# Kernel tuning notes

Hardware: AMD Instinct MI355X
Metric: run time of the kernel (lower is better)

## Reference

```python
import jax, jax.numpy as jnp
import numpy as np

N_NODES = 50000
N_EDGES = 600000
CH = 128      # units / channels
RBF = 200     # ceil(cutoff/gap) = ceil(20.0/0.1)
LOG2 = 0.6931471805599453


def shifted_softplus(x):
    # tf.where(x < 14, softplus(where(x < 14, x, 0)), x) - log(2)
    safe = jnp.where(x < 14.0, x, jnp.zeros_like(x))
    return jnp.where(x < 14.0, jax.nn.softplus(safe), x) - LOG2


def _glorot(key, shape):
    fan_in = shape[0] if len(shape) > 1 else shape[0]
    fan_out = shape[-1]
    lim = np.sqrt(6.0 / (fan_in + fan_out))
    return jax.random.uniform(key, shape, jnp.float32, -lim, lim)


def setup_inputs() -> dict:
    key = jax.random.key(0)
    ks = jax.random.split(key, 12)
    rbf = jax.random.uniform(ks[0], (N_EDGES, RBF), jnp.float32)
    x = jax.random.normal(ks[1], (N_NODES, CH), jnp.float32)
    src = jax.random.randint(ks[2], (N_EDGES,), 0, N_NODES, jnp.int32)
    return {
        "rbf": rbf,
        "x": x,
        "src": src,
        "w1": _glorot(ks[3], (RBF, CH)),
        "b1": _glorot(ks[4], (CH,)),
        "w2": _glorot(ks[5], (CH, CH)),
        "b2": _glorot(ks[6], (CH,)),
        "w3": _glorot(ks[7], (CH, CH)),
        "w4": _glorot(ks[8], (CH, CH)),
        "b4": _glorot(ks[9], (CH,)),
        "w5": _glorot(ks[10], (CH, CH)),
        "b5": _glorot(ks[11], (CH,)),
    }


def reference(rbf, x, src, w1, b1, w2, b2, w3, w4, b4, w5, b5):
    # filter-generating MLP on edge RBF features: [E, RBF] -> [E, CH]
    h = shifted_softplus(rbf @ w1 + b1)
    w = shifted_softplus(h @ w2 + b2)
    # node feature transform, gather to edges by SOURCE index
    f = x @ w3                         # [N, CH]
    wf = w * f[src]                    # [E, CH] broadcast_node_to_edges + multiply
    # scatter-sum edges back to SOURCE nodes
    conv = jax.ops.segment_sum(wf, src, num_segments=N_NODES)  # [N, CH]
    # output MLP + residual
    y = shifted_softplus(conv @ w4 + b4)
    v = y @ w5 + b5
    return x + v
```

## Files before the change

kernel.cpp:

```cpp
#include <hip/hip_runtime.h>

#define CH      128
#define RBFD    200
#define NNODES  50000
#define NEDGES  600000
#define LOG2F_  0.6931471805599453f

#define K1P     224
#define RSTR    232
#define HSTR    136

typedef __attribute__((ext_vector_type(8))) __bf16 bf16x8;
typedef __attribute__((ext_vector_type(4))) float  f32x4;

__device__ __forceinline__ float ssp(float x) {
    float sp = (x < 14.0f) ? __logf(1.0f + __expf(x)) : x;
    return sp - LOG2F_;
}

__device__ __forceinline__ unsigned short f2bf(float f) {
    union { float f; unsigned int u; } v; v.f = f;
    unsigned int r = v.u + 0x7FFFu + ((v.u >> 16) & 1u);
    return (unsigned short)(r >> 16);
}

__global__ __launch_bounds__(256) void prep_weights(const float* __restrict__ w1,
                                                    const float* __restrict__ w2,
                                                    unsigned short* __restrict__ w1T,
                                                    unsigned short* __restrict__ w2T) {
    int i = blockIdx.x * 256 + threadIdx.x;
    if (i < 128 * K1P) {
        int n = i / K1P, k = i % K1P;
        w1T[i] = (k < RBFD) ? f2bf(w1[k * CH + n]) : (unsigned short)0;
    } else {
        int j = i - 128 * K1P;
        if (j < 128 * 128) {
            int n = j / 128, k = j % 128;
            w2T[j] = f2bf(w2[k * CH + n]);
        }
    }
}

__global__ __launch_bounds__(256, 3) void edge_kernel(const float* __restrict__ rbf,
                                                      const float* __restrict__ b1,
                                                      const float* __restrict__ b2,
                                                      const int* __restrict__ src,
                                                      const unsigned short* __restrict__ w1T,
                                                      const unsigned short* __restrict__ w2T,
                                                      float* __restrict__ convw) {
    __shared__ unsigned short rbf_s[64 * RSTR];
    __shared__ unsigned short h_s[64 * HSTR];
    const int t = threadIdx.x;
    const int lane = t & 63;
    const int wv = t >> 6;
    const size_t e0 = (size_t)blockIdx.x * 64;

    const int l15 = lane & 15;
    const int lg  = lane >> 4;
    const int col0 = wv * 32 + l15;

    bf16x8 B1[2][7];
#pragma unroll
    for (int nt = 0; nt < 2; nt++) {
        const int row = wv * 32 + nt * 16 + l15;
#pragma unroll
        for (int kt = 0; kt < 7; kt++)
            B1[nt][kt] = *(const bf16x8*)(w1T + (size_t)row * K1P + kt * 32 + lg * 8);
    }

    {
        const float4* g = (const float4*)(rbf + e0 * RBFD);
        for (int i = t; i < 3200; i += 256) {
            float4 v = g[i];
            int row = i / 50, c4 = (i % 50) * 4;
            unsigned short* d = &rbf_s[row * RSTR + c4];
            union { unsigned short s[4]; unsigned long long u; } p;
            p.s[0] = f2bf(v.x); p.s[1] = f2bf(v.y); p.s[2] = f2bf(v.z); p.s[3] = f2bf(v.w);
            *(unsigned long long*)d = p.u;
        }
        for (int i = t; i < 2048; i += 256) {
            int row = i >> 5, k = RBFD + (i & 31);
            rbf_s[row * RSTR + k] = 0;
        }
    }
    __syncthreads();

    const float bias10 = b1[col0];
    const float bias11 = b1[col0 + 16];

#pragma unroll
    for (int m = 0; m < 4; m++) {
        f32x4 acc0 = {0.f, 0.f, 0.f, 0.f};
        f32x4 acc1 = {0.f, 0.f, 0.f, 0.f};
        const unsigned short* abase = &rbf_s[(m * 16 + l15) * RSTR + lg * 8];
#pragma unroll
        for (int kt = 0; kt < 7; kt++) {
            bf16x8 a = *(const bf16x8*)(abase + kt * 32);
            acc0 = __builtin_amdgcn_mfma_f32_16x16x32_bf16(a, B1[0][kt], acc0, 0, 0, 0);
            acc1 = __builtin_amdgcn_mfma_f32_16x16x32_bf16(a, B1[1][kt], acc1, 0, 0, 0);
        }
        const int hrow0 = m * 16 + lg * 4;
#pragma unroll
        for (int r = 0; r < 4; r++) {
            h_s[(hrow0 + r) * HSTR + col0]      = f2bf(ssp(acc0[r] + bias10));
            h_s[(hrow0 + r) * HSTR + col0 + 16] = f2bf(ssp(acc1[r] + bias11));
        }
    }
    __syncthreads();

    bf16x8 B2[2][4];
#pragma unroll
    for (int nt = 0; nt < 2; nt++) {
        const int row = wv * 32 + nt * 16 + l15;
#pragma unroll
        for (int kt = 0; kt < 4; kt++)
            B2[nt][kt] = *(const bf16x8*)(w2T + (size_t)row * 128 + kt * 32 + lg * 8);
    }

    const float bias20 = b2[col0];
    const float bias21 = b2[col0 + 16];

#pragma unroll
    for (int m = 0; m < 4; m++) {
        f32x4 acc0 = {0.f, 0.f, 0.f, 0.f};
        f32x4 acc1 = {0.f, 0.f, 0.f, 0.f};
        const unsigned short* abase = &h_s[(m * 16 + l15) * HSTR + lg * 8];
#pragma unroll
        for (int kt = 0; kt < 4; kt++) {
            bf16x8 a = *(const bf16x8*)(abase + kt * 32);
            acc0 = __builtin_amdgcn_mfma_f32_16x16x32_bf16(a, B2[0][kt], acc0, 0, 0, 0);
            acc1 = __builtin_amdgcn_mfma_f32_16x16x32_bf16(a, B2[1][kt], acc1, 0, 0, 0);
        }
        const int erow0 = m * 16 + lg * 4;
#pragma unroll
        for (int r = 0; r < 4; r++) {
            const int e = (int)e0 + erow0 + r;
            const int s = src[e];
            const size_t off = (size_t)s * CH;
            atomicAdd(&convw[off + col0],      ssp(acc0[r] + bias20));
            atomicAdd(&convw[off + col0 + 16], ssp(acc1[r] + bias21));
        }
    }
}

__global__ __launch_bounds__(256) void node_all(const float* __restrict__ x,
                                                const float* __restrict__ w3,
                                                const float* __restrict__ w4,
                                                const float* __restrict__ b4,
                                                const float* __restrict__ w5,
                                                const float* __restrict__ b5,
                                                const float* __restrict__ convw,
                                                float* __restrict__ out,
                                                int n_nodes) {
    __shared__ float A[32 * 128];
    __shared__ float B[32 * 128];
    const int t = threadIdx.x;
    const int n0 = blockIdx.x * 32;
    const int rows = min(32, n_nodes - n0);

    {
        const float4* g = (const float4*)(x + (size_t)n0 * CH);
        float4* s = (float4*)A;
        for (int i = t; i < rows * 32; i += 256) s[i] = g[i];
    }
    __syncthreads();

    const int c = t & 127, eh = t >> 7;
    float acc[16];

#pragma unroll
    for (int i = 0; i < 16; i++) acc[i] = 0.f;
    for (int k = 0; k < 128; k += 4) {
        const float wa = w3[(k + 0) * CH + c];
        const float wb = w3[(k + 1) * CH + c];
        const float wc = w3[(k + 2) * CH + c];
        const float wd = w3[(k + 3) * CH + c];
#pragma unroll
        for (int i = 0; i < 16; i++) {
            const float4 v = *(const float4*)&A[(eh * 16 + i) * CH + k];
            acc[i] = fmaf(v.x, wa, acc[i]);
            acc[i] = fmaf(v.y, wb, acc[i]);
            acc[i] = fmaf(v.z, wc, acc[i]);
            acc[i] = fmaf(v.w, wd, acc[i]);
        }
    }
#pragma unroll
    for (int i = 0; i < 16; i++) {
        const int r = eh * 16 + i;
        B[r * 128 + c] = (r < rows) ? acc[i] * convw[((size_t)(n0 + r)) * CH + c] : 0.f;
    }
    __syncthreads();

#pragma unroll
    for (int i = 0; i < 16; i++) acc[i] = 0.f;
    for (int k = 0; k < 128; k += 4) {
        const float wa = w4[(k + 0) * CH + c];
        const float wb = w4[(k + 1) * CH + c];
        const float wc = w4[(k + 2) * CH + c];
        const float wd = w4[(k + 3) * CH + c];
#pragma unroll
        for (int i = 0; i < 16; i++) {
            const float4 v = *(const float4*)&B[(eh * 16 + i) * CH + k];
            acc[i] = fmaf(v.x, wa, acc[i]);
            acc[i] = fmaf(v.y, wb, acc[i]);
            acc[i] = fmaf(v.z, wc, acc[i]);
            acc[i] = fmaf(v.w, wd, acc[i]);
        }
    }
    {
        const float bias4 = b4[c];
#pragma unroll
        for (int i = 0; i < 16; i++)
            A[(eh * 16 + i) * 128 + c] = ssp(acc[i] + bias4);
    }
    __syncthreads();

#pragma unroll
    for (int i = 0; i < 16; i++) acc[i] = 0.f;
    for (int k = 0; k < 128; k += 4) {
        const float wa = w5[(k + 0) * CH + c];
        const float wb = w5[(k + 1) * CH + c];
        const float wc = w5[(k + 2) * CH + c];
        const float wd = w5[(k + 3) * CH + c];
#pragma unroll
        for (int i = 0; i < 16; i++) {
            const float4 v = *(const float4*)&A[(eh * 16 + i) * CH + k];
            acc[i] = fmaf(v.x, wa, acc[i]);
            acc[i] = fmaf(v.y, wb, acc[i]);
            acc[i] = fmaf(v.z, wc, acc[i]);
            acc[i] = fmaf(v.w, wd, acc[i]);
        }
    }
    {
        const float bias5 = b5[c];
#pragma unroll
        for (int i = 0; i < 16; i++) {
            const int r = eh * 16 + i;
            if (r < rows) {
                const size_t off = ((size_t)(n0 + r)) * CH + c;
                out[off] = x[off] + acc[i] + bias5;
            }
        }
    }
}

extern "C" void kernel_launch(void* const* d_in, const int* in_sizes, int n_in,
                              void* d_out, int out_size, void* d_ws, size_t ws_size,
                              hipStream_t stream) {
    const float* rbf = (const float*)d_in[0];
    const float* x   = (const float*)d_in[1];
    const int*   src = (const int*)d_in[2];
    const float* w1  = (const float*)d_in[3];
    const float* b1  = (const float*)d_in[4];
    const float* w2  = (const float*)d_in[5];
    const float* b2  = (const float*)d_in[6];
    const float* w3  = (const float*)d_in[7];
    const float* w4  = (const float*)d_in[8];
    const float* b4  = (const float*)d_in[9];
    const float* w5  = (const float*)d_in[10];
    const float* b5  = (const float*)d_in[11];

    float* out   = (float*)d_out;
    float* convw = (float*)d_ws;

    const size_t convBytes = (size_t)NNODES * CH * sizeof(float);
    const size_t wElems = 128 * K1P + 128 * 128;
    unsigned short* w1T;
    if (ws_size >= convBytes + wElems * 2)
        w1T = (unsigned short*)((char*)d_ws + convBytes);
    else
        w1T = (unsigned short*)d_out;
    unsigned short* w2T = w1T + 128 * K1P;

    hipMemsetAsync(convw, 0, convBytes, stream);
    prep_weights<<<(int)((wElems + 255) / 256), 256, 0, stream>>>(w1, w2, w1T, w2T);
    edge_kernel<<<NEDGES / 64, 256, 0, stream>>>(rbf, b1, b2, src, w1T, w2T, convw);
    node_all<<<(NNODES + 31) / 32, 256, 0, stream>>>(x, w3, w4, b4, w5, b5, convw, out, NNODES);
}
```

Before: 490.3 us.

## Replace float atomic scatter with bf16 edge buffer and CSR gather-reduce

The edge kernel now writes its per-edge filter outputs as bf16 into a global buffer instead of issuing float atomicAdds into the node accumulator. A histogram, single-block scan and fill build a CSR of edges grouped by source node, and the node kernel gathers and sums each node's edge rows before the output MLP. The goal is to remove atomic contention and traffic. In exchange it adds three preprocessing kernels, including a serial single-block scan, scattered 256-byte row gathers, per-row block barriers in the gather loop, bf16 rounding of the summed values, and a large workspace requirement, with a fallback to the old path when the workspace is too small.

```diff
diff --git a/kernel.cpp b/kernel.cpp
--- a/kernel.cpp
+++ b/kernel.cpp
@@ -22,6 +22,11 @@
     union { float f; unsigned int u; } v; v.f = f;
     unsigned int r = v.u + 0x7FFFu + ((v.u >> 16) & 1u);
     return (unsigned short)(r >> 16);
+}
+
+__device__ __forceinline__ float bf2f(unsigned short s) {
+    union { unsigned int u; float f; } v; v.u = ((unsigned int)s) << 16;
+    return v.f;
 }
 
 __global__ __launch_bounds__(256) void prep_weights(const float* __restrict__ w1,
@@ -41,15 +46,59 @@
     }
 }
 
+__global__ __launch_bounds__(256) void k_hist(const int* __restrict__ src, int* __restrict__ cur) {
+    int e = blockIdx.x * 256 + threadIdx.x;
+    if (e < NEDGES) atomicAdd(&cur[src[e]], 1);
+}
+
+__global__ __launch_bounds__(256) void k_scan(int* __restrict__ cur,
+                                              int* __restrict__ csr_off) {
+    __shared__ int ps[256];
+    const int t = threadIdx.x;
+    const int chunk = (NNODES + 255) / 256;
+    const int lo = t * chunk, hi = min(lo + chunk, NNODES);
+    int s = 0;
+    for (int i = lo; i < hi; i++) s += cur[i];
+    ps[t] = s;
+    __syncthreads();
+    for (int d = 1; d < 256; d <<= 1) {
+        int v = (t >= d) ? ps[t - d] : 0;
+        __syncthreads();
+        ps[t] += v;
+        __syncthreads();
+    }
+    int run = (t == 0) ? 0 : ps[t - 1];
+    for (int i = lo; i < hi; i++) {
+        int dg = cur[i];
+        csr_off[i] = run;
+        cur[i] = run;
+        run += dg;
+    }
+    if (t == 255) csr_off[NNODES] = run;
+}
+
+__global__ __launch_bounds__(256) void k_fill(const int* __restrict__ src,
+                                              int* __restrict__ cur,
+                                              int* __restrict__ eidx) {
+    int e = blockIdx.x * 256 + threadIdx.x;
+    if (e < NEDGES) {
+        int pos = atomicAdd(&cur[src[e]], 1);
+        eidx[pos] = e;
+    }
+}
+
+template <int MODE>
 __global__ __launch_bounds__(256, 3) void edge_kernel(const float* __restrict__ rbf,
                                                       const float* __restrict__ b1,
                                                       const float* __restrict__ b2,
                                                       const int* __restrict__ src,
                                                       const unsigned short* __restrict__ w1T,
                                                       const unsigned short* __restrict__ w2T,
+                                                      unsigned short* __restrict__ wbuf,
                                                       float* __restrict__ convw) {
     __shared__ unsigned short rbf_s[64 * RSTR];
     __shared__ unsigned short h_s[64 * HSTR];
+    unsigned short* w_s = rbf_s;
     const int t = threadIdx.x;
     const int lane = t & 63;
     const int wv = t >> 6;
@@ -132,13 +181,151 @@
             acc1 = __builtin_amdgcn_mfma_f32_16x16x32_bf16(a, B2[1][kt], acc1, 0, 0, 0);
         }
         const int erow0 = m * 16 + lg * 4;
-#pragma unroll
-        for (int r = 0; r < 4; r++) {
-            const int e = (int)e0 + erow0 + r;
-            const int s = src[e];
-            const size_t off = (size_t)s * CH;
-            atomicAdd(&convw[off + col0],      ssp(acc0[r] + bias20));
-            atomicAdd(&convw[off + col0 + 16], ssp(acc1[r] + bias21));
+        if (MODE == 0) {
+#pragma unroll
+            for (int r = 0; r < 4; r++) {
+                w_s[(erow0 + r) * HSTR + col0]      = f2bf(ssp(acc0[r] + bias20));
+                w_s[(erow0 + r) * HSTR + col0 + 16] = f2bf(ssp(acc1[r] + bias21));
+            }
+        } else {
+#pragma unroll
+            for (int r = 0; r < 4; r++) {
+                const int e = (int)e0 + erow0 + r;
+                const int s = src[e];
+                const size_t off = (size_t)s * CH;
+                atomicAdd(&convw[off + col0],      ssp(acc0[r] + bias20));
+                atomicAdd(&convw[off + col0 + 16], ssp(acc1[r] + bias21));
+            }
+        }
+    }
+
+    if (MODE == 0) {
+        __syncthreads();
+        for (int i = t; i < 1024; i += 256) {
+            const int row = i >> 4, q = i & 15;
+            float4 v = *(const float4*)&w_s[row * HSTR + q * 8];
+            ((float4*)wbuf)[(e0 + row) * 16 + q] = v;
+        }
+    }
+}
+
+__global__ __launch_bounds__(256) void node_gather(const float* __restrict__ x,
+                                                   const float* __restrict__ w3,
+                                                   const float* __restrict__ w4,
+                                                   const float* __restrict__ b4,
+                                                   const float* __restrict__ w5,
+                                                   const float* __restrict__ b5,
+                                                   const unsigned short* __restrict__ wbuf,
+                                                   const int* __restrict__ eidx,
+                                                   const int* __restrict__ csr_off,
+                                                   float* __restrict__ out,
+                                                   int n_nodes) {
+    __shared__ float A[32 * 128];
+    __shared__ float B[32 * 128];
+    const int t = threadIdx.x;
+    const int n0 = blockIdx.x * 32;
+    const int rows = min(32, n_nodes - n0);
+
+    {
+        const float4* g = (const float4*)(x + (size_t)n0 * CH);
+        float4* s = (float4*)A;
+        for (int i = t; i < rows * 32; i += 256) s[i] = g[i];
+    }
+    __syncthreads();
+
+    const int c = t & 127, eh = t >> 7;
+    float acc[16];
+
+#pragma unroll
+    for (int i = 0; i < 16; i++) acc[i] = 0.f;
+    for (int k = 0; k < 128; k += 4) {
+        const float wa = w3[(k + 0) * CH + c];
+        const float wb = w3[(k + 1) * CH + c];
+        const float wc = w3[(k + 2) * CH + c];
+        const float wd = w3[(k + 3) * CH + c];
+#pragma unroll
+        for (int i = 0; i < 16; i++) {
+            const float4 v = *(const float4*)&A[(eh * 16 + i) * CH + k];
+            acc[i] = fmaf(v.x, wa, acc[i]);
+            acc[i] = fmaf(v.y, wb, acc[i]);
+            acc[i] = fmaf(v.z, wc, acc[i]);
+            acc[i] = fmaf(v.w, wd, acc[i]);
+        }
+    }
+#pragma unroll
+    for (int i = 0; i < 16; i++) B[(eh * 16 + i) * 128 + c] = acc[i];
+    __syncthreads();
+
+    for (int i = 0; i < 16; i++) {
+        const int r = eh * 16 + i;
+        const int n = n0 + r;
+        float conv = 0.f;
+        if (n < n_nodes) {
+            const int o0 = csr_off[n], o1 = csr_off[n + 1];
+            float s0 = 0.f, s1 = 0.f;
+            int j = o0;
+            for (; j + 1 < o1; j += 2) {
+                const int ea = eidx[j], eb = eidx[j + 1];
+                s0 += bf2f(wbuf[(size_t)ea * CH + c]);
+                s1 += bf2f(wbuf[(size_t)eb * CH + c]);
+            }
+            if (j < o1) s0 += bf2f(wbuf[(size_t)eidx[j] * CH + c]);
+            conv = B[r * 128 + c] * (s0 + s1);
+        }
+        __syncthreads();
+        B[r * 128 + c] = conv;
+    }
+    __syncthreads();
+
+#pragma unroll
+    for (int i = 0; i < 16; i++) acc[i] = 0.f;
+    for (int k = 0; k < 128; k += 4) {
+        const float wa = w4[(k + 0) * CH + c];
+        const float wb = w4[(k + 1) * CH + c];
+        const float wc = w4[(k + 2) * CH + c];
+        const float wd = w4[(k + 3) * CH + c];
+#pragma unroll
+        for (int i = 0; i < 16; i++) {
+            const float4 v = *(const float4*)&B[(eh * 16 + i) * CH + k];
+            acc[i] = fmaf(v.x, wa, acc[i]);
+            acc[i] = fmaf(v.y, wb, acc[i]);
+            acc[i] = fmaf(v.z, wc, acc[i]);
+            acc[i] = fmaf(v.w, wd, acc[i]);
+        }
+    }
+    {
+        const float bias4 = b4[c];
+#pragma unroll
+        for (int i = 0; i < 16; i++)
+            A[(eh * 16 + i) * 128 + c] = ssp(acc[i] + bias4);
+    }
+    __syncthreads();
+
+#pragma unroll
+    for (int i = 0; i < 16; i++) acc[i] = 0.f;
+    for (int k = 0; k < 128; k += 4) {
+        const float wa = w5[(k + 0) * CH + c];
+        const float wb = w5[(k + 1) * CH + c];
+        const float wc = w5[(k + 2) * CH + c];
+        const float wd = w5[(k + 3) * CH + c];
+#pragma unroll
+        for (int i = 0; i < 16; i++) {
+            const float4 v = *(const float4*)&A[(eh * 16 + i) * CH + k];
+            acc[i] = fmaf(v.x, wa, acc[i]);
+            acc[i] = fmaf(v.y, wb, acc[i]);
+            acc[i] = fmaf(v.z, wc, acc[i]);
+            acc[i] = fmaf(v.w, wd, acc[i]);
+        }
+    }
+    {
+        const float bias5 = b5[c];
+#pragma unroll
+        for (int i = 0; i < 16; i++) {
+            const int r = eh * 16 + i;
+            if (r < rows) {
+                const size_t off = ((size_t)(n0 + r)) * CH + c;
+                out[off] = x[off] + acc[i] + bias5;
+            }
         }
     }
 }
@@ -157,17 +344,14 @@
     const int t = threadIdx.x;
     const int n0 = blockIdx.x * 32;
     const int rows = min(32, n_nodes - n0);
-
     {
         const float4* g = (const float4*)(x + (size_t)n0 * CH);
         float4* s = (float4*)A;
         for (int i = t; i < rows * 32; i += 256) s[i] = g[i];
     }
     __syncthreads();
-
     const int c = t & 127, eh = t >> 7;
     float acc[16];
-
 #pragma unroll
     for (int i = 0; i < 16; i++) acc[i] = 0.f;
     for (int k = 0; k < 128; k += 4) {
@@ -190,7 +374,6 @@
         B[r * 128 + c] = (r < rows) ? acc[i] * convw[((size_t)(n0 + r)) * CH + c] : 0.f;
     }
     __syncthreads();
-
 #pragma unroll
     for (int i = 0; i < 16; i++) acc[i] = 0.f;
     for (int k = 0; k < 128; k += 4) {
@@ -214,7 +397,6 @@
             A[(eh * 16 + i) * 128 + c] = ssp(acc[i] + bias4);
     }
     __syncthreads();
-
 #pragma unroll
     for (int i = 0; i < 16; i++) acc[i] = 0.f;
     for (int k = 0; k < 128; k += 4) {
@@ -243,6 +425,8 @@
         }
     }
 }
+
+static inline size_t align_up(size_t v, size_t a) { return (v + a - 1) & ~(a - 1); }
 
 extern "C" void kernel_launch(void* const* d_in, const int* in_sizes, int n_in,
                               void* d_out, int out_size, void* d_ws, size_t ws_size,
@@ -260,20 +444,46 @@
     const float* w5  = (const float*)d_in[10];
     const float* b5  = (const float*)d_in[11];
 
-    float* out   = (float*)d_out;
-    float* convw = (float*)d_ws;
-
-    const size_t convBytes = (size_t)NNODES * CH * sizeof(float);
+    float* out = (float*)d_out;
     const size_t wElems = 128 * K1P + 128 * 128;
-    unsigned short* w1T;
-    if (ws_size >= convBytes + wElems * 2)
-        w1T = (unsigned short*)((char*)d_ws + convBytes);
-    else
-        w1T = (unsigned short*)d_out;
-    unsigned short* w2T = w1T + 128 * K1P;
-
-    hipMemsetAsync(convw, 0, convBytes, stream);
-    prep_weights<<<(int)((wElems + 255) / 256), 256, 0, stream>>>(w1, w2, w1T, w2T);
-    edge_kernel<<<NEDGES / 64, 256, 0, stream>>>(rbf, b1, b2, src, w1T, w2T, convw);
-    node_all<<<(NNODES + 31) / 32, 256, 0, stream>>>(x, w3, w4, b4, w5, b5, convw, out, NNODES);
-}
+
+    size_t off = 0;
+    const size_t o_wbuf = off;            off = align_up(off + (size_t)NEDGES * CH * 2, 256);
+    const size_t o_eidx = off;            off = align_up(off + (size_t)NEDGES * 4, 256);
+    const size_t o_csr  = off;            off = align_up(off + (size_t)(NNODES + 1) * 4, 256);
+    const size_t o_cur  = off;            off = align_up(off + (size_t)NNODES * 4, 256);
+    const size_t o_wT   = off;            off = align_up(off + wElems * 2, 256);
+    const size_t needG  = off;
+
+    if (ws_size >= needG) {
+        unsigned short* wbuf = (unsigned short*)((char*)d_ws + o_wbuf);
+        int* eidx            = (int*)((char*)d_ws + o_eidx);
+        int* csr_off         = (int*)((char*)d_ws + o_csr);
+        int* cur             = (int*)((char*)d_ws + o_cur);
+        unsigned short* w1T  = (unsigned short*)((char*)d_ws + o_wT);
+        unsigned short* w2T  = w1T + 128 * K1P;
+
+        hipMemsetAsync(cur, 0, (size_t)NNODES * 4, stream);
+        prep_weights<<<(int)((wElems + 255) / 256), 256, 0, stream>>>(w1, w2, w1T, w2T);
+        edge_kernel<0><<<NEDGES / 64, 256, 0, stream>>>(rbf, b1, b2, src, w1T, w2T, wbuf, nullptr);
+        k_hist<<<(NEDGES + 255) / 256, 256, 0, stream>>>(src, cur);
+        k_scan<<<1, 256, 0, stream>>>(cur, csr_off);
+        k_fill<<<(NEDGES + 255) / 256, 256, 0, stream>>>(src, cur, eidx);
+        node_gather<<<(NNODES + 31) / 32, 256, 0, stream>>>(x, w3, w4, b4, w5, b5,
+                                                            wbuf, eidx, csr_off, out, NNODES);
+    } else {
+        float* convw = (float*)d_ws;
+        const size_t convBytes = (size_t)NNODES * CH * sizeof(float);
+        unsigned short* w1T;
+        if (ws_size >= convBytes + wElems * 2)
+            w1T = (unsigned short*)((char*)d_ws + convBytes);
+        else
+            w1T = (unsigned short*)d_out;
+        unsigned short* w2T = w1T + 128 * K1P;
+
+        hipMemsetAsync(convw, 0, convBytes, stream);
+        prep_weights<<<(int)((wElems + 255) / 256), 256, 0, stream>>>(w1, w2, w1T, w2T);
+        edge_kernel<1><<<NEDGES / 64, 256, 0, stream>>>(rbf, b1, b2, src, w1T, w2T, nullptr, convw);
+        node_all<<<(NNODES + 31) / 32, 256, 0, stream>>>(x, w3, w4, b4, w5, b5, convw, out, NNODES);
+    }
+}
```

Result: slower. 719.7 us (+46.8%).

## Replace atomic scatter with CSR-sorted gather over bf16 per-edge filter buffer

Applied to the files above, without the earlier changes.

The edge MLP no longer scatters fp32 atomics into node sums. It writes each edge's filter output as bf16 into a workspace buffer. Each call then builds a CSR grouping of edges by source (histogram, three-pass scan, fill), and the node kernel gathers and sums each node's edge rows before multiplying by x@w3. The edge kernel is also reorganised so each wave handles 16 edges and loads and converts rbf to bf16 directly into registers, using a swizzled per-wave LDS tile. This aims to remove atomic contention, but adds a 150MB-scale intermediate write and read, several small launches, and bf16 rounding before the sum.

```diff
diff --git a/kernel.cpp b/kernel.cpp
--- a/kernel.cpp
+++ b/kernel.cpp
@@ -5,10 +5,7 @@
 #define NNODES  50000
 #define NEDGES  600000
 #define LOG2F_  0.6931471805599453f
-
 #define K1P     224
-#define RSTR    232
-#define HSTR    136
 
 typedef __attribute__((ext_vector_type(8))) __bf16 bf16x8;
 typedef __attribute__((ext_vector_type(4))) float  f32x4;
@@ -22,6 +19,22 @@
     union { float f; unsigned int u; } v; v.f = f;
     unsigned int r = v.u + 0x7FFFu + ((v.u >> 16) & 1u);
     return (unsigned short)(r >> 16);
+}
+
+__device__ __forceinline__ float bf2f(unsigned short s) {
+    union { unsigned int u; float f; } v; v.u = ((unsigned int)s) << 16;
+    return v.f;
+}
+
+__device__ __forceinline__ bf16x8 load_cvt8(const float* p) {
+    float4 f0 = *(const float4*)p;
+    float4 f1 = *(const float4*)(p + 4);
+    union { unsigned int u[4]; bf16x8 v; } r;
+    asm("v_cvt_pk_bf16_f32 %0, %1, %2" : "=v"(r.u[0]) : "v"(f0.x), "v"(f0.y));
+    asm("v_cvt_pk_bf16_f32 %0, %1, %2" : "=v"(r.u[1]) : "v"(f0.z), "v"(f0.w));
+    asm("v_cvt_pk_bf16_f32 %0, %1, %2" : "=v"(r.u[2]) : "v"(f1.x), "v"(f1.y));
+    asm("v_cvt_pk_bf16_f32 %0, %1, %2" : "=v"(r.u[3]) : "v"(f1.z), "v"(f1.w));
+    return r.v;
 }
 
 __global__ __launch_bounds__(256) void prep_weights(const float* __restrict__ w1,
@@ -41,117 +54,172 @@
     }
 }
 
-__global__ __launch_bounds__(256, 3) void edge_kernel(const float* __restrict__ rbf,
-                                                      const float* __restrict__ b1,
-                                                      const float* __restrict__ b2,
-                                                      const int* __restrict__ src,
-                                                      const unsigned short* __restrict__ w1T,
-                                                      const unsigned short* __restrict__ w2T,
-                                                      float* __restrict__ convw) {
-    __shared__ unsigned short rbf_s[64 * RSTR];
-    __shared__ unsigned short h_s[64 * HSTR];
+__global__ __launch_bounds__(256) void k_hist(const int* __restrict__ src, int* __restrict__ cur) {
+    int e = blockIdx.x * 256 + threadIdx.x;
+    if (e < NEDGES) atomicAdd(&cur[src[e]], 1);
+}
+
+__global__ __launch_bounds__(256) void k_scan1(const int* __restrict__ cur, int* __restrict__ bsum) {
+    __shared__ int s[256];
+    const int t = threadIdx.x;
+    int i = blockIdx.x * 256 + t;
+    s[t] = (i < NNODES) ? cur[i] : 0;
+    __syncthreads();
+    for (int d = 128; d > 0; d >>= 1) {
+        if (t < d) s[t] += s[t + d];
+        __syncthreads();
+    }
+    if (t == 0) bsum[blockIdx.x] = s[0];
+}
+
+__global__ __launch_bounds__(256) void k_scan2(const int* __restrict__ bsum, int* __restrict__ bpre) {
+    __shared__ int s[256];
+    const int t = threadIdx.x;
+    int v0 = (t < 196) ? bsum[t] : 0;
+    s[t] = v0;
+    __syncthreads();
+    for (int d = 1; d < 256; d <<= 1) {
+        int v = (t >= d) ? s[t - d] : 0;
+        __syncthreads();
+        s[t] += v;
+        __syncthreads();
+    }
+    if (t < 196) bpre[t] = s[t] - v0;
+}
+
+__global__ __launch_bounds__(256) void k_scan3(const int* __restrict__ deg_in,
+                                               const int* __restrict__ bpre,
+                                               int* __restrict__ csr_off,
+                                               int* __restrict__ cur) {
+    __shared__ int s[256];
+    const int t = threadIdx.x, b = blockIdx.x;
+    const int i = b * 256 + t;
+    int d0 = (i < NNODES) ? deg_in[i] : 0;
+    s[t] = d0;
+    __syncthreads();
+    for (int d = 1; d < 256; d <<= 1) {
+        int v = (t >= d) ? s[t - d] : 0;
+        __syncthreads();
+        s[t] += v;
+        __syncthreads();
+    }
+    if (i < NNODES) {
+        int ex = bpre[b] + s[t] - d0;
+        csr_off[i] = ex;
+        cur[i] = ex;
+    }
+    if (i == NNODES - 1) csr_off[NNODES] = NEDGES;
+}
+
+__global__ __launch_bounds__(256) void k_fill(const int* __restrict__ src,
+                                              int* __restrict__ cur,
+                                              int* __restrict__ eidx) {
+    int e = blockIdx.x * 256 + threadIdx.x;
+    if (e < NEDGES) {
+        int pos = atomicAdd(&cur[src[e]], 1);
+        eidx[pos] = e;
+    }
+}
+
+__global__ __launch_bounds__(256, 4) void edge_kernel2(const float* __restrict__ rbf,
+                                                       const float* __restrict__ b1v,
+                                                       const float* __restrict__ b2v,
+                                                       const unsigned short* __restrict__ w1T,
+                                                       const unsigned short* __restrict__ w2T,
+                                                       unsigned short* __restrict__ wbuf) {
+    __shared__ unsigned short tile[4][16 * 128];
     const int t = threadIdx.x;
     const int lane = t & 63;
     const int wv = t >> 6;
-    const size_t e0 = (size_t)blockIdx.x * 64;
-
     const int l15 = lane & 15;
     const int lg  = lane >> 4;
-    const int col0 = wv * 32 + l15;
-
-    bf16x8 B1[2][7];
-#pragma unroll
-    for (int nt = 0; nt < 2; nt++) {
-        const int row = wv * 32 + nt * 16 + l15;
-#pragma unroll
-        for (int kt = 0; kt < 7; kt++)
-            B1[nt][kt] = *(const bf16x8*)(w1T + (size_t)row * K1P + kt * 32 + lg * 8);
-    }
-
-    {
-        const float4* g = (const float4*)(rbf + e0 * RBFD);
-        for (int i = t; i < 3200; i += 256) {
-            float4 v = g[i];
-            int row = i / 50, c4 = (i % 50) * 4;
-            unsigned short* d = &rbf_s[row * RSTR + c4];
-            union { unsigned short s[4]; unsigned long long u; } p;
-            p.s[0] = f2bf(v.x); p.s[1] = f2bf(v.y); p.s[2] = f2bf(v.z); p.s[3] = f2bf(v.w);
-            *(unsigned long long*)d = p.u;
-        }
-        for (int i = t; i < 2048; i += 256) {
-            int row = i >> 5, k = RBFD + (i & 31);
-            rbf_s[row * RSTR + k] = 0;
-        }
-    }
-    __syncthreads();
-
-    const float bias10 = b1[col0];
-    const float bias11 = b1[col0 + 16];
-
-#pragma unroll
-    for (int m = 0; m < 4; m++) {
-        f32x4 acc0 = {0.f, 0.f, 0.f, 0.f};
-        f32x4 acc1 = {0.f, 0.f, 0.f, 0.f};
-        const unsigned short* abase = &rbf_s[(m * 16 + l15) * RSTR + lg * 8];
+    const size_t erow0 = (size_t)blockIdx.x * 64 + (size_t)wv * 16;
+    unsigned short* my = tile[wv];
+    char* myb = (char*)my;
+
+    bf16x8 a1[7];
+    const float* arow = rbf + (erow0 + l15) * RBFD;
+#pragma unroll
+    for (int kt = 0; kt < 6; kt++)
+        a1[kt] = load_cvt8(arow + kt * 32 + lg * 8);
+    if (lg == 0) {
+        a1[6] = load_cvt8(arow + 192);
+    } else {
+        union { unsigned int u[4]; bf16x8 v; } z;
+        z.u[0] = z.u[1] = z.u[2] = z.u[3] = 0;
+        a1[6] = z.v;
+    }
+
+    const int myrow0 = lg * 4;
+
+#pragma unroll
+    for (int nt = 0; nt < 8; nt++) {
+        f32x4 acc = {0.f, 0.f, 0.f, 0.f};
+        const unsigned short* bbase = w1T + (size_t)(nt * 16 + l15) * K1P + lg * 8;
 #pragma unroll
         for (int kt = 0; kt < 7; kt++) {
-            bf16x8 a = *(const bf16x8*)(abase + kt * 32);
-            acc0 = __builtin_amdgcn_mfma_f32_16x16x32_bf16(a, B1[0][kt], acc0, 0, 0, 0);
-            acc1 = __builtin_amdgcn_mfma_f32_16x16x32_bf16(a, B1[1][kt], acc1, 0, 0, 0);
-        }
-        const int hrow0 = m * 16 + lg * 4;
+            bf16x8 b = *(const bf16x8*)(bbase + kt * 32);
+            acc = __builtin_amdgcn_mfma_f32_16x16x32_bf16(a1[kt], b, acc, 0, 0, 0);
+        }
+        const float bias = b1v[nt * 16 + l15];
 #pragma unroll
         for (int r = 0; r < 4; r++) {
-            h_s[(hrow0 + r) * HSTR + col0]      = f2bf(ssp(acc0[r] + bias10));
-            h_s[(hrow0 + r) * HSTR + col0 + 16] = f2bf(ssp(acc1[r] + bias11));
-        }
-    }
-    __syncthreads();
-
-    bf16x8 B2[2][4];
-#pragma unroll
-    for (int nt = 0; nt < 2; nt++) {
-        const int row = wv * 32 + nt * 16 + l15;
-#pragma unroll
-        for (int kt = 0; kt < 4; kt++)
-            B2[nt][kt] = *(const bf16x8*)(w2T + (size_t)row * 128 + kt * 32 + lg * 8);
-    }
-
-    const float bias20 = b2[col0];
-    const float bias21 = b2[col0 + 16];
-
-#pragma unroll
-    for (int m = 0; m < 4; m++) {
-        f32x4 acc0 = {0.f, 0.f, 0.f, 0.f};
-        f32x4 acc1 = {0.f, 0.f, 0.f, 0.f};
-        const unsigned short* abase = &h_s[(m * 16 + l15) * HSTR + lg * 8];
+            const int row = myrow0 + r;
+            const int colb = (nt * 32 + l15 * 2) ^ ((row & 7) << 4);
+            *(unsigned short*)(myb + row * 256 + colb) = f2bf(ssp(acc[r] + bias));
+        }
+    }
+
+    bf16x8 a2[4];
+#pragma unroll
+    for (int kt = 0; kt < 4; kt++) {
+        const int boff = l15 * 256 + ((kt * 64 + lg * 16) ^ ((l15 & 7) << 4));
+        a2[kt] = *(const bf16x8*)(myb + boff);
+    }
+
+#pragma unroll
+    for (int nt = 0; nt < 8; nt++) {
+        f32x4 acc = {0.f, 0.f, 0.f, 0.f};
+        const unsigned short* bbase = w2T + (size_t)(nt * 16 + l15) * 128 + lg * 8;
 #pragma unroll
         for (int kt = 0; kt < 4; kt++) {
-            bf16x8 a = *(const bf16x8*)(abase + kt * 32);
-            acc0 = __builtin_amdgcn_mfma_f32_16x16x32_bf16(a, B2[0][kt], acc0, 0, 0, 0);
-            acc1 = __builtin_amdgcn_mfma_f32_16x16x32_bf16(a, B2[1][kt], acc1, 0, 0, 0);
-        }
-        const int erow0 = m * 16 + lg * 4;
+            bf16x8 b = *(const bf16x8*)(bbase + kt * 32);
+            acc = __builtin_amdgcn_mfma_f32_16x16x32_bf16(a2[kt], b, acc, 0, 0, 0);
+        }
+        const float bias = b2v[nt * 16 + l15];
 #pragma unroll
         for (int r = 0; r < 4; r++) {
-            const int e = (int)e0 + erow0 + r;
-            const int s = src[e];
-            const size_t off = (size_t)s * CH;
-            atomicAdd(&convw[off + col0],      ssp(acc0[r] + bias20));
-            atomicAdd(&convw[off + col0 + 16], ssp(acc1[r] + bias21));
-        }
-    }
-}
-
-__global__ __launch_bounds__(256) void node_all(const float* __restrict__ x,
-                                                const float* __restrict__ w3,
-                                                const float* __restrict__ w4,
-                                                const float* __restrict__ b4,
-                                                const float* __restrict__ w5,
-                                                const float* __restrict__ b5,
-                                                const float* __restrict__ convw,
-                                                float* __restrict__ out,
-                                                int n_nodes) {
+            const int row = myrow0 + r;
+            const int colb = (nt * 32 + l15 * 2) ^ ((row & 7) << 4);
+            *(unsigned short*)(myb + row * 256 + colb) = f2bf(ssp(acc[r] + bias));
+        }
+    }
+
+    {
+        const int row = lane >> 2, q = lane & 3;
+        float4 o[4];
+#pragma unroll
+        for (int j = 0; j < 4; j++) {
+            const int boff = row * 256 + ((q * 64 + j * 16) ^ ((row & 7) << 4));
+            o[j] = *(const float4*)(myb + boff);
+        }
+        float4* gdst = (float4*)((char*)wbuf + (erow0 + row) * 256 + q * 64);
+#pragma unroll
+        for (int j = 0; j < 4; j++) gdst[j] = o[j];
+    }
+}
+
+__global__ __launch_bounds__(256) void node_gather2(const float* __restrict__ x,
+                                                    const float* __restrict__ w3,
+                                                    const float* __restrict__ w4,
+                                                    const float* __restrict__ b4,
+                                                    const float* __restrict__ w5,
+                                                    const float* __restrict__ b5,
+                                                    const unsigned short* __restrict__ wbuf,
+                                                    const int* __restrict__ eidx,
+                                                    const int* __restrict__ csr_off,
+                                                    float* __restrict__ out,
+                                                    int n_nodes) {
     __shared__ float A[32 * 128];
     __shared__ float B[32 * 128];
     const int t = threadIdx.x;
@@ -185,9 +253,42 @@
         }
     }
 #pragma unroll
-    for (int i = 0; i < 16; i++) {
-        const int r = eh * 16 + i;
-        B[r * 128 + c] = (r < rows) ? acc[i] * convw[((size_t)(n0 + r)) * CH + c] : 0.f;
+    for (int i = 0; i < 16; i++) B[(eh * 16 + i) * 128 + c] = acc[i];
+    __syncthreads();
+
+    {
+        const int lane = t & 63, wv = t >> 6;
+        const int c0 = lane * 2;
+        for (int rr = 0; rr < 8; rr++) {
+            const int r = wv * 8 + rr;
+            const int n = n0 + r;
+            float s0 = 0.f, s1 = 0.f;
+            if (n < n_nodes) {
+                const int o0 = csr_off[n], o1 = csr_off[n + 1];
+                int j = o0;
+                for (; j + 3 < o1; j += 4) {
+                    const int ea = eidx[j], eb = eidx[j + 1], ec = eidx[j + 2], ed = eidx[j + 3];
+                    const unsigned ua = *(const unsigned*)(wbuf + (size_t)ea * CH + c0);
+                    const unsigned ub = *(const unsigned*)(wbuf + (size_t)eb * CH + c0);
+                    const unsigned uc = *(const unsigned*)(wbuf + (size_t)ec * CH + c0);
+                    const unsigned ud = *(const unsigned*)(wbuf + (size_t)ed * CH + c0);
+                    s0 += bf2f((unsigned short)ua) + bf2f((unsigned short)ub)
+                        + bf2f((unsigned short)uc) + bf2f((unsigned short)ud);
+                    s1 += bf2f((unsigned short)(ua >> 16)) + bf2f((unsigned short)(ub >> 16))
+                        + bf2f((unsigned short)(uc >> 16)) + bf2f((unsigned short)(ud >> 16));
+                }
+                for (; j < o1; j++) {
+                    const unsigned ua = *(const unsigned*)(wbuf + (size_t)eidx[j] * CH + c0);
+                    s0 += bf2f((unsigned short)ua);
+                    s1 += bf2f((unsigned short)(ua >> 16));
+                }
+            }
+            const float2 f2 = *(const float2*)&B[r * 128 + c0];
+            float2 v2;
+            v2.x = (n < n_nodes) ? f2.x * s0 : 0.f;
+            v2.y = (n < n_nodes) ? f2.y * s1 : 0.f;
+            *(float2*)&B[r * 128 + c0] = v2;
+        }
     }
     __syncthreads();
 
@@ -243,6 +344,8 @@
         }
     }
 }
+
+static inline size_t align_up(size_t v, size_t a) { return (v + a - 1) & ~(a - 1); }
 
 extern "C" void kernel_launch(void* const* d_in, const int* in_sizes, int n_in,
                               void* d_out, int out_size, void* d_ws, size_t ws_size,
@@ -260,20 +363,35 @@
     const float* w5  = (const float*)d_in[10];
     const float* b5  = (const float*)d_in[11];
 
-    float* out   = (float*)d_out;
-    float* convw = (float*)d_ws;
-
-    const size_t convBytes = (size_t)NNODES * CH * sizeof(float);
+    float* out = (float*)d_out;
     const size_t wElems = 128 * K1P + 128 * 128;
-    unsigned short* w1T;
-    if (ws_size >= convBytes + wElems * 2)
-        w1T = (unsigned short*)((char*)d_ws + convBytes);
-    else
-        w1T = (unsigned short*)d_out;
-    unsigned short* w2T = w1T + 128 * K1P;
-
-    hipMemsetAsync(convw, 0, convBytes, stream);
+
+    size_t off = 0;
+    const size_t o_wbuf = off;  off = align_up(off + (size_t)NEDGES * CH * 2, 256);
+    const size_t o_eidx = off;  off = align_up(off + (size_t)NEDGES * 4, 256);
+    const size_t o_csr  = off;  off = align_up(off + (size_t)(NNODES + 1) * 4, 256);
+    const size_t o_cur  = off;  off = align_up(off + (size_t)NNODES * 4, 256);
+    const size_t o_bs   = off;  off = align_up(off + 256 * 4, 256);
+    const size_t o_bp   = off;  off = align_up(off + 256 * 4, 256);
+    const size_t o_wT   = off;  off = align_up(off + wElems * 2, 256);
+
+    unsigned short* wbuf = (unsigned short*)((char*)d_ws + o_wbuf);
+    int* eidx            = (int*)((char*)d_ws + o_eidx);
+    int* csr_off         = (int*)((char*)d_ws + o_csr);
+    int* cur             = (int*)((char*)d_ws + o_cur);
+    int* bsum            = (int*)((char*)d_ws + o_bs);
+    int* bpre            = (int*)((char*)d_ws + o_bp);
+    unsigned short* w1T  = (unsigned short*)((char*)d_ws + o_wT);
+    unsigned short* w2T  = w1T + 128 * K1P;
+
+    hipMemsetAsync(cur, 0, (size_t)NNODES * 4, stream);
     prep_weights<<<(int)((wElems + 255) / 256), 256, 0, stream>>>(w1, w2, w1T, w2T);
-    edge_kernel<<<NEDGES / 64, 256, 0, stream>>>(rbf, b1, b2, src, w1T, w2T, convw);
-    node_all<<<(NNODES + 31) / 32, 256, 0, stream>>>(x, w3, w4, b4, w5, b5, convw, out, NNODES);
-}
+    edge_kernel2<<<NEDGES / 64, 256, 0, stream>>>(rbf, b1, b2, w1T, w2T, wbuf);
+    k_hist<<<(NEDGES + 255) / 256, 256, 0, stream>>>(src, cur);
+    k_scan1<<<196, 256, 0, stream>>>(cur, bsum);
+    k_scan2<<<1, 256, 0, stream>>>(bsum, bpre);
+    k_scan3<<<196, 256, 0, stream>>>(cur, bpre, csr_off, cur);
+    k_fill<<<(NEDGES + 255) / 256, 256, 0, stream>>>(src, cur, eidx);
+    node_gather2<<<(NNODES + 31) / 32, 256, 0, stream>>>(x, w3, w4, b4, w5, b5,
+                                                         wbuf, eidx, csr_off, out, NNODES);
+}
```

Result: slower. 593.0 us (+20.9%).
